# Kernel tuning notes

Hardware: AMD Instinct MI355X
Metric: run time of the kernel (lower is better)

## Reference

```python
import jax, jax.numpy as jnp
import numpy as np

TEMP = 0.07


def setup_inputs() -> dict:
    key = jax.random.key(0)
    k1, k2 = jax.random.split(key)
    B, m, d = 256, 128, 768
    v_final = jax.random.normal(k1, (B, d), dtype=jnp.float32)
    T_fused = jax.random.normal(k2, (B, m, d), dtype=jnp.float32)
    return {"v_final": v_final, "T_fused": T_fused}


def reference(v_final, T_fused):
    B = v_final.shape[0]
    # [B, B, m] token-level similarities, scaled by temperature
    sim = jnp.einsum('id,jmd->ijm', v_final, T_fused) / TEMP
    # max over text tokens (ColBERT max-sim) -> [B, B]
    sim_max = sim.max(axis=-1)
    targets = jnp.arange(B)
    # symmetric cross-entropy with diagonal targets
    logp_i2t = jax.nn.log_softmax(sim_max, axis=-1)
    logp_t2i = jax.nn.log_softmax(sim_max.T, axis=-1)
    loss_i2t = -jnp.mean(logp_i2t[targets, targets])
    loss_t2i = -jnp.mean(logp_t2i[targets, targets])
    return (loss_i2t + loss_t2i) / 2
```

## Files before the change

kernel.cpp:

```cpp
#include <hip/hip_runtime.h>
#include <hip/hip_bf16.h>

constexpr int BATCH = 256;
constexpr int MTOK  = 128;
constexpr int DDIM  = 768;
constexpr int NV    = BATCH * DDIM;
constexpr float INV_TEMP = 1.0f / 0.07f;

typedef __bf16 bf16;
typedef __bf16 bf16x8 __attribute__((ext_vector_type(8)));
typedef float  f32x4  __attribute__((ext_vector_type(4)));

__global__ __launch_bounds__(256) void pack_v_kernel(
        const float* __restrict__ V, bf16x8* __restrict__ Vq) {
    int c = blockIdx.x * 256 + threadIdx.x;
    int lane = c & 63, fs = c >> 6;
    int ks = fs % 24, g = fs / 24;
    int l15 = lane & 15, quad = lane >> 4;
    const float* src = V + (size_t)(g * 16 + l15) * DDIM + ks * 32 + quad * 8;
    float4 f0 = *(const float4*)(src);
    float4 f1 = *(const float4*)(src + 4);
    bf16x8 o;
    o[0] = (bf16)f0.x; o[1] = (bf16)f0.y; o[2] = (bf16)f0.z; o[3] = (bf16)f0.w;
    o[4] = (bf16)f1.x; o[5] = (bf16)f1.y; o[6] = (bf16)f1.z; o[7] = (bf16)f1.w;
    Vq[c] = o;
}

__global__ __launch_bounds__(256, 4) void gemm_max_kernel(
        const bf16*  __restrict__ Vq,
        const float* __restrict__ T,
        float* __restrict__ Sp) {
    __shared__ char  ldsB[2 * 4096];
    __shared__ float smax[256];

    const int jt   = blockIdx.x >> 2;
    const int nh   = blockIdx.x & 3;
    const int tid  = threadIdx.x;
    const int w    = tid >> 6;
    const int lane = tid & 63;
    const int quad = lane >> 4;
    const int l15  = lane & 15;

    const bf16* aBase[4];
#pragma unroll
    for (int t = 0; t < 4; ++t)
        aBase[t] = Vq + ((size_t)(w * 4 + t) * 24) * 512 + lane * 8;

    const int brow = tid >> 3, bkp = tid & 7;
    const float* gB = T + (size_t)(jt * MTOK + nh * 32 + brow) * DDIM + bkp * 8;
    const int bwoff = (bkp >> 2) * 2048 + brow * 64 + (((bkp & 3) ^ (brow & 3)) << 4);

    int boff[2][2];
#pragma unroll
    for (int h = 0; h < 2; ++h)
#pragma unroll
        for (int tc = 0; tc < 2; ++tc) {
            int br = tc * 16 + l15;
            boff[h][tc] = h * 2048 + br * 64 + ((quad ^ (l15 & 3)) << 4);
        }

    f32x4 acc[4][2] = {};

    auto cvt_store = [&](float4 a, float4 b, int bufo) {
        bf16x8 o;
        o[0] = (bf16)a.x; o[1] = (bf16)a.y; o[2] = (bf16)a.z; o[3] = (bf16)a.w;
        o[4] = (bf16)b.x; o[5] = (bf16)b.y; o[6] = (bf16)b.z; o[7] = (bf16)b.w;
        *(bf16x8*)(ldsB + bufo + bwoff) = o;
    };

    {
        float4 r0 = *(const float4*)(gB);
        float4 r1 = *(const float4*)(gB + 4);
        cvt_store(r0, r1, 0);
    }
    float4 breg0 = *(const float4*)(gB + 64);
    float4 breg1 = *(const float4*)(gB + 64 + 4);
    bf16x8 apre[4];
#pragma unroll
    for (int t = 0; t < 4; ++t) apre[t] = *(const bf16x8*)(aBase[t]);
    __syncthreads();

    for (int kk = 0; kk < 12; ++kk) {
        const int buf  = (kk & 1) * 4096;
        const int nbuf = buf ^ 4096;
        if (kk < 11) cvt_store(breg0, breg1, nbuf);
        if (kk < 10) {
            const float* p = gB + (kk + 2) * 64;
            breg0 = *(const float4*)(p);
            breg1 = *(const float4*)(p + 4);
        }
#pragma unroll
        for (int h = 0; h < 2; ++h) {
            const int hs = kk * 2 + h;
            bf16x8 af[4], bb[2];
#pragma unroll
            for (int t = 0; t < 4; ++t) af[t] = apre[t];
            if (hs < 23) {
#pragma unroll
                for (int t = 0; t < 4; ++t)
                    apre[t] = *(const bf16x8*)(aBase[t] + (size_t)(hs + 1) * 512);
            }
#pragma unroll
            for (int tc = 0; tc < 2; ++tc)
                bb[tc] = *(const bf16x8*)(ldsB + buf + boff[h][tc]);
#pragma unroll
            for (int tr = 0; tr < 4; ++tr)
#pragma unroll
                for (int tc = 0; tc < 2; ++tc)
                    acc[tr][tc] = __builtin_amdgcn_mfma_f32_16x16x32_bf16(
                        af[tr], bb[tc], acc[tr][tc], 0, 0, 0);
        }
        __syncthreads();
    }

#pragma unroll
    for (int tr = 0; tr < 4; ++tr) {
#pragma unroll
        for (int r = 0; r < 4; ++r) {
            float v = fmaxf(acc[tr][0][r], acc[tr][1][r]);
            v = fmaxf(v, __shfl_xor(v, 1, 64));
            v = fmaxf(v, __shfl_xor(v, 2, 64));
            v = fmaxf(v, __shfl_xor(v, 4, 64));
            v = fmaxf(v, __shfl_xor(v, 8, 64));
            if (l15 == 0)
                smax[w * 64 + tr * 16 + quad * 4 + r] = v;
        }
    }
    __syncthreads();
    Sp[((size_t)nh * BATCH + jt) * BATCH + tid] = smax[tid] * INV_TEMP;
}

__global__ __launch_bounds__(64) void ce1_kernel(
        const float* __restrict__ Sp, float* __restrict__ partial) {
    const int t = blockIdx.x;
    const int l = threadIdx.x;
    const int P = BATCH * BATCH;

    float vr[4], vc[4];
#pragma unroll
    for (int p = 0; p < 4; ++p) {
        int j = p * 64 + l;
        float a = fmaxf(Sp[0 * P + j * BATCH + t], Sp[1 * P + j * BATCH + t]);
        float b = fmaxf(Sp[2 * P + j * BATCH + t], Sp[3 * P + j * BATCH + t]);
        vr[p] = fmaxf(a, b);
        int i = p * 64 + l;
        float c = fmaxf(Sp[0 * P + t * BATCH + i], Sp[1 * P + t * BATCH + i]);
        float d = fmaxf(Sp[2 * P + t * BATCH + i], Sp[3 * P + t * BATCH + i]);
        vc[p] = fmaxf(c, d);
    }
    float mr = fmaxf(fmaxf(vr[0], vr[1]), fmaxf(vr[2], vr[3]));
    float mc = fmaxf(fmaxf(vc[0], vc[1]), fmaxf(vc[2], vc[3]));
    for (int o = 32; o > 0; o >>= 1) {
        mr = fmaxf(mr, __shfl_xor(mr, o, 64));
        mc = fmaxf(mc, __shfl_xor(mc, o, 64));
    }
    float sr = 0.f, sc = 0.f;
#pragma unroll
    for (int p = 0; p < 4; ++p) {
        sr += expf(vr[p] - mr);
        sc += expf(vc[p] - mc);
    }
    for (int o = 32; o > 0; o >>= 1) {
        sr += __shfl_xor(sr, o, 64);
        sc += __shfl_xor(sc, o, 64);
    }
    if (l == 0) {
        float d0 = fmaxf(Sp[0 * P + t * BATCH + t], Sp[1 * P + t * BATCH + t]);
        float d1 = fmaxf(Sp[2 * P + t * BATCH + t], Sp[3 * P + t * BATCH + t]);
        partial[t] = 0.5f * ((mr + logf(sr)) + (mc + logf(sc))) - fmaxf(d0, d1);
    }
}

__global__ __launch_bounds__(256) void ce2_kernel(
        const float* __restrict__ partial, float* __restrict__ out) {
    const int i = threadIdx.x;
    float term = partial[i];
    for (int o = 32; o > 0; o >>= 1) term += __shfl_down(term, o, 64);
    __shared__ float ps[4];
    if ((i & 63) == 0) ps[i >> 6] = term;
    __syncthreads();
    if (i == 0) out[0] = (ps[0] + ps[1] + ps[2] + ps[3]) / (float)BATCH;
}

extern "C" void kernel_launch(void* const* d_in, const int* in_sizes, int n_in,
                              void* d_out, int out_size, void* d_ws, size_t ws_size,
                              hipStream_t stream) {
    const float* v = (const float*)d_in[0];
    const float* T = (const float*)d_in[1];

    bf16*  Vq = (bf16*)d_ws;
    float* Sp = (float*)((char*)d_ws + (size_t)NV * sizeof(bf16));
    float* partial = Sp + 4 * BATCH * BATCH;

    pack_v_kernel<<<96, 256, 0, stream>>>(v, (bf16x8*)Vq);
    gemm_max_kernel<<<1024, 256, 0, stream>>>(Vq, T, Sp);
    ce1_kernel<<<256, 64, 0, stream>>>(Sp, partial);
    ce2_kernel<<<1, 256, 0, stream>>>(partial, (float*)d_out);
}
```

Baseline: 171.6 us.

## Double GEMM N-tile to 64 tokens per block, halving V reloads

Each gemm_max block now handles 64 text tokens instead of 32, with a 4x4 MFMA accumulator tile and a doubled LDS buffer. The grid shrinks from 1024 to 512 blocks, so each block re-reads the bf16 V operand half as often. The A prefetch is made two stages deep, and the partial-max buffer and ce1 reduction drop from 4 to 2 slices. In exchange, register use grows, the occupancy hint drops to 2, and the LDS XOR swizzle is removed, which may cause bank conflicts.

```diff
diff --git a/kernel.cpp b/kernel.cpp
--- a/kernel.cpp
+++ b/kernel.cpp
@@ -26,15 +26,15 @@
     Vq[c] = o;
 }
 
-__global__ __launch_bounds__(256, 4) void gemm_max_kernel(
+__global__ __launch_bounds__(256, 2) void gemm_max_kernel(
         const bf16*  __restrict__ Vq,
         const float* __restrict__ T,
         float* __restrict__ Sp) {
-    __shared__ char  ldsB[2 * 4096];
+    __shared__ char  ldsB[2 * 8192];
     __shared__ float smax[256];
 
-    const int jt   = blockIdx.x >> 2;
-    const int nh   = blockIdx.x & 3;
+    const int jt   = blockIdx.x >> 1;
+    const int nh   = blockIdx.x & 1;
     const int tid  = threadIdx.x;
     const int w    = tid >> 6;
     const int lane = tid & 63;
@@ -46,67 +46,83 @@
     for (int t = 0; t < 4; ++t)
         aBase[t] = Vq + ((size_t)(w * 4 + t) * 24) * 512 + lane * 8;
 
-    const int brow = tid >> 3, bkp = tid & 7;
-    const float* gB = T + (size_t)(jt * MTOK + nh * 32 + brow) * DDIM + bkp * 8;
-    const int bwoff = (bkp >> 2) * 2048 + brow * 64 + (((bkp & 3) ^ (brow & 3)) << 4);
-
-    int boff[2][2];
+    const float* gB[2];
+    int bwoff[2];
+#pragma unroll
+    for (int q = 0; q < 2; ++q) {
+        int c = q * 256 + tid;
+        int row = c >> 3, kp = c & 7;
+        gB[q] = T + (size_t)(jt * MTOK + nh * 64 + row) * DDIM + kp * 8;
+        bwoff[q] = (kp >> 2) * 4096 + row * 64 + ((kp & 3) << 4);
+    }
+
+    int boff[2][4];
 #pragma unroll
     for (int h = 0; h < 2; ++h)
 #pragma unroll
-        for (int tc = 0; tc < 2; ++tc) {
-            int br = tc * 16 + l15;
-            boff[h][tc] = h * 2048 + br * 64 + ((quad ^ (l15 & 3)) << 4);
-        }
-
-    f32x4 acc[4][2] = {};
-
-    auto cvt_store = [&](float4 a, float4 b, int bufo) {
+        for (int tc = 0; tc < 4; ++tc)
+            boff[h][tc] = h * 4096 + (tc * 16 + l15) * 64 + quad * 16;
+
+    f32x4 acc[4][4] = {};
+
+    auto cvt_store = [&](float4 a, float4 b, int q, int bufo) {
         bf16x8 o;
         o[0] = (bf16)a.x; o[1] = (bf16)a.y; o[2] = (bf16)a.z; o[3] = (bf16)a.w;
         o[4] = (bf16)b.x; o[5] = (bf16)b.y; o[6] = (bf16)b.z; o[7] = (bf16)b.w;
-        *(bf16x8*)(ldsB + bufo + bwoff) = o;
+        *(bf16x8*)(ldsB + bufo + bwoff[q]) = o;
     };
 
-    {
-        float4 r0 = *(const float4*)(gB);
-        float4 r1 = *(const float4*)(gB + 4);
-        cvt_store(r0, r1, 0);
-    }
-    float4 breg0 = *(const float4*)(gB + 64);
-    float4 breg1 = *(const float4*)(gB + 64 + 4);
-    bf16x8 apre[4];
-#pragma unroll
-    for (int t = 0; t < 4; ++t) apre[t] = *(const bf16x8*)(aBase[t]);
+    float4 breg[2][2];
+#pragma unroll
+    for (int q = 0; q < 2; ++q) {
+        float4 r0 = *(const float4*)(gB[q]);
+        float4 r1 = *(const float4*)(gB[q] + 4);
+        cvt_store(r0, r1, q, 0);
+        breg[q][0] = *(const float4*)(gB[q] + 64);
+        breg[q][1] = *(const float4*)(gB[q] + 64 + 4);
+    }
+    bf16x8 apre[2][4];
+#pragma unroll
+    for (int h = 0; h < 2; ++h)
+#pragma unroll
+        for (int t = 0; t < 4; ++t)
+            apre[h][t] = *(const bf16x8*)(aBase[t] + (size_t)h * 512);
     __syncthreads();
 
     for (int kk = 0; kk < 12; ++kk) {
-        const int buf  = (kk & 1) * 4096;
-        const int nbuf = buf ^ 4096;
-        if (kk < 11) cvt_store(breg0, breg1, nbuf);
+        const int buf  = (kk & 1) * 8192;
+        const int nbuf = buf ^ 8192;
+        if (kk < 11) {
+#pragma unroll
+            for (int q = 0; q < 2; ++q)
+                cvt_store(breg[q][0], breg[q][1], q, nbuf);
+        }
         if (kk < 10) {
-            const float* p = gB + (kk + 2) * 64;
-            breg0 = *(const float4*)(p);
-            breg1 = *(const float4*)(p + 4);
+#pragma unroll
+            for (int q = 0; q < 2; ++q) {
+                const float* p = gB[q] + (kk + 2) * 64;
+                breg[q][0] = *(const float4*)(p);
+                breg[q][1] = *(const float4*)(p + 4);
+            }
         }
 #pragma unroll
         for (int h = 0; h < 2; ++h) {
             const int hs = kk * 2 + h;
-            bf16x8 af[4], bb[2];
-#pragma unroll
-            for (int t = 0; t < 4; ++t) af[t] = apre[t];
-            if (hs < 23) {
+            bf16x8 af[4], bb[4];
+#pragma unroll
+            for (int t = 0; t < 4; ++t) af[t] = apre[h][t];
+            if (hs + 2 < 24) {
 #pragma unroll
                 for (int t = 0; t < 4; ++t)
-                    apre[t] = *(const bf16x8*)(aBase[t] + (size_t)(hs + 1) * 512);
+                    apre[h][t] = *(const bf16x8*)(aBase[t] + (size_t)(hs + 2) * 512);
             }
 #pragma unroll
-            for (int tc = 0; tc < 2; ++tc)
+            for (int tc = 0; tc < 4; ++tc)
                 bb[tc] = *(const bf16x8*)(ldsB + buf + boff[h][tc]);
 #pragma unroll
             for (int tr = 0; tr < 4; ++tr)
 #pragma unroll
-                for (int tc = 0; tc < 2; ++tc)
+                for (int tc = 0; tc < 4; ++tc)
                     acc[tr][tc] = __builtin_amdgcn_mfma_f32_16x16x32_bf16(
                         af[tr], bb[tc], acc[tr][tc], 0, 0, 0);
         }
@@ -117,7 +133,8 @@
     for (int tr = 0; tr < 4; ++tr) {
 #pragma unroll
         for (int r = 0; r < 4; ++r) {
-            float v = fmaxf(acc[tr][0][r], acc[tr][1][r]);
+            float v = fmaxf(fmaxf(acc[tr][0][r], acc[tr][1][r]),
+                            fmaxf(acc[tr][2][r], acc[tr][3][r]));
             v = fmaxf(v, __shfl_xor(v, 1, 64));
             v = fmaxf(v, __shfl_xor(v, 2, 64));
             v = fmaxf(v, __shfl_xor(v, 4, 64));
@@ -134,19 +151,16 @@
         const float* __restrict__ Sp, float* __restrict__ partial) {
     const int t = blockIdx.x;
     const int l = threadIdx.x;
-    const int P = BATCH * BATCH;
+    const float* Sp0 = Sp;
+    const float* Sp1 = Sp + BATCH * BATCH;
 
     float vr[4], vc[4];
 #pragma unroll
     for (int p = 0; p < 4; ++p) {
         int j = p * 64 + l;
-        float a = fmaxf(Sp[0 * P + j * BATCH + t], Sp[1 * P + j * BATCH + t]);
-        float b = fmaxf(Sp[2 * P + j * BATCH + t], Sp[3 * P + j * BATCH + t]);
-        vr[p] = fmaxf(a, b);
+        vr[p] = fmaxf(Sp0[j * BATCH + t], Sp1[j * BATCH + t]);
         int i = p * 64 + l;
-        float c = fmaxf(Sp[0 * P + t * BATCH + i], Sp[1 * P + t * BATCH + i]);
-        float d = fmaxf(Sp[2 * P + t * BATCH + i], Sp[3 * P + t * BATCH + i]);
-        vc[p] = fmaxf(c, d);
+        vc[p] = fmaxf(Sp0[t * BATCH + i], Sp1[t * BATCH + i]);
     }
     float mr = fmaxf(fmaxf(vr[0], vr[1]), fmaxf(vr[2], vr[3]));
     float mc = fmaxf(fmaxf(vc[0], vc[1]), fmaxf(vc[2], vc[3]));
@@ -165,9 +179,8 @@
         sc += __shfl_xor(sc, o, 64);
     }
     if (l == 0) {
-        float d0 = fmaxf(Sp[0 * P + t * BATCH + t], Sp[1 * P + t * BATCH + t]);
-        float d1 = fmaxf(Sp[2 * P + t * BATCH + t], Sp[3 * P + t * BATCH + t]);
-        partial[t] = 0.5f * ((mr + logf(sr)) + (mc + logf(sc))) - fmaxf(d0, d1);
+        float diag = fmaxf(Sp0[t * BATCH + t], Sp1[t * BATCH + t]);
+        partial[t] = 0.5f * ((mr + logf(sr)) + (mc + logf(sc))) - diag;
     }
 }
 
@@ -190,10 +203,10 @@
 
     bf16*  Vq = (bf16*)d_ws;
     float* Sp = (float*)((char*)d_ws + (size_t)NV * sizeof(bf16));
-    float* partial = Sp + 4 * BATCH * BATCH;
+    float* partial = Sp + 2 * BATCH * BATCH;
 
     pack_v_kernel<<<96, 256, 0, stream>>>(v, (bf16x8*)Vq);
-    gemm_max_kernel<<<1024, 256, 0, stream>>>(Vq, T, Sp);
+    gemm_max_kernel<<<512, 256, 0, stream>>>(Vq, T, Sp);
     ce1_kernel<<<256, 64, 0, stream>>>(Sp, partial);
     ce2_kernel<<<1, 256, 0, stream>>>(partial, (float*)d_out);
 }
```

New measurement: 163.5 us. 4.7% less time.
